# Performance work log

Measured on AMD Instinct MI355X. Metric: run time of the kernel, lower is better.

The kernel has to match this reference:

```python
import jax, jax.numpy as jnp
import numpy as np

EPS = 1e-12  # F.normalize clamp


def setup_inputs() -> dict:
    key = jax.random.key(0)
    features = jax.random.normal(key, (8192, 256), dtype=jnp.float32)
    return {"features": features}


def reference(features) -> jnp.ndarray:
    # F.normalize(features, dim=1)
    norm = jnp.maximum(jnp.linalg.norm(features, axis=1, keepdims=True), EPS)
    f = features / norm
    sim = f @ f.T  # [2B, 2B]
    n = sim.shape[0]
    b = n // 2
    idx = jnp.arange(n)
    # positive pair index: idx+B for first half, idx-B for second half
    pos_idx = jnp.where(idx < b, idx + b, idx - b)
    pos = sim[idx, pos_idx]  # sim with the positive example
    # CE with target 0 over logits row [pos, negatives (all j != i, j != pos)]:
    # denominator = exp(pos) + sum_{j != i, j != pos} exp(sim_ij) = sum_{j != i} exp(sim_ij)
    self_mask = idx[:, None] == idx[None, :]
    masked = jnp.where(self_mask, -jnp.inf, sim)
    lse = jax.nn.logsumexp(masked, axis=1)
    loss = jnp.mean(lse - pos)
    return loss
```

## Files before the change

### kernel.cpp

```cpp
#include <hip/hip_runtime.h>
#include <hip/hip_bf16.h>
#include <stdint.h>

#define N 8192
#define D 256
#define ROWB 256
#define COLG 16
#define COLS_PER_BLK (N / COLG)
#define CTILE 32
#define NT (COLS_PER_BLK / CTILE)
#define TILE_BYTES (CTILE * D)
#define NBUF 4
#define E_CONST 2.71828182845904523536f

typedef __attribute__((ext_vector_type(4))) int i32x4;
typedef __attribute__((ext_vector_type(8))) int i32x8;
typedef __attribute__((ext_vector_type(16))) float f32x16;

typedef const __attribute__((address_space(1))) void gvoid_t;
typedef __attribute__((address_space(3))) void lvoid_t;
__device__ inline void gload_lds16(const void* g, void* l) {
  __builtin_amdgcn_global_load_lds((gvoid_t*)g, (lvoid_t*)l, 16, 0, 0);
}

#if !__has_builtin(__builtin_amdgcn_cvt_pk_fp8_f32)
__device__ inline unsigned int f2e4m3(float x) {
  union { float f; unsigned u; } c; c.f = x;
  unsigned s = (c.u >> 31) << 7;
  float ax = fabsf(x);
  if (!(ax > 0.0f)) return s;
  if (ax >= 448.0f) return s | 0x7E;
  int e; float m = frexpf(ax, &e);
  int E = e - 1 + 7;
  if (E <= 0) {
    int qi = (int)rintf(ax * 512.0f);
    if (qi > 7) return s | 0x08;
    return s | (unsigned)qi;
  }
  int qi = (int)rintf(m * 16.0f);
  if (qi == 16) { qi = 8; E += 1; }
  if (E > 15) return s | 0x7E;
  return s | (unsigned)((E << 3) | (qi - 8));
}
#endif

__global__ __launch_bounds__(256) void norm_kernel(const float* __restrict__ feat,
                                                   unsigned char* __restrict__ f8,
                                                   float* __restrict__ pos,
                                                   float* __restrict__ out) {
  __shared__ float4 sh[4][64];
  int wave = threadIdx.x >> 6, lane = threadIdx.x & 63;
  int base = blockIdx.x << 1;
  int row = (wave < 2) ? (base + wave) : (4096 + base + (wave - 2));
  const float4 v = *(const float4*)(feat + (size_t)row * D + lane * 4);
  float ss = v.x * v.x + v.y * v.y + v.z * v.z + v.w * v.w;
  for (int m = 1; m < 64; m <<= 1) ss += __shfl_xor(ss, m, 64);
  float rn = 1.0f / fmaxf(sqrtf(ss), 1e-12f);
  float4 nv = make_float4(v.x * rn, v.y * rn, v.z * rn, v.w * rn);
#if __has_builtin(__builtin_amdgcn_cvt_pk_fp8_f32)
  int p = __builtin_amdgcn_cvt_pk_fp8_f32(nv.x, nv.y, 0, 0);
  p = __builtin_amdgcn_cvt_pk_fp8_f32(nv.z, nv.w, p, 1);
#else
  int p = (int)(f2e4m3(nv.x) | (f2e4m3(nv.y) << 8) |
                (f2e4m3(nv.z) << 16) | (f2e4m3(nv.w) << 24));
#endif
  *(int*)(f8 + (size_t)row * D + lane * 4) = p;
  sh[wave][lane] = nv;
  __syncthreads();
  if (wave < 2) {
    float4 q = sh[wave + 2][lane];
    float d = nv.x * q.x + nv.y * q.y + nv.z * q.z + nv.w * q.w;
    for (int m = 1; m < 64; m <<= 1) d += __shfl_xor(d, m, 64);
    if (lane == 0) {
      pos[base + wave] = d;
      pos[4096 + base + wave] = d;
    }
  }
  if (blockIdx.x == 0 && threadIdx.x == 0) out[0] = 0.0f;
}

__global__ __launch_bounds__(512, 4) void simlse_kernel(const unsigned char* __restrict__ f8,
                                                        float* __restrict__ slab) {
  __shared__ char lds[NBUF * TILE_BYTES];
  const char* fb = (const char*)f8;
  int tid = threadIdx.x;
  int wave = tid >> 6, lane = tid & 63;
  int c31 = lane & 31, h = lane >> 5;
  int rb = blockIdx.x >> 4;
  int cg = blockIdx.x & 15;
  int rowbase = rb * ROWB + wave * 32;

  i32x8 a[4];
  {
    const char* ar = fb + (size_t)(rowbase + c31) * D + h * 32;
#pragma unroll
    for (int m = 0; m < 4; ++m) {
      i32x4 lo = *(const i32x4*)(ar + m * 64);
      i32x4 hi = *(const i32x4*)(ar + m * 64 + 16);
      a[m] = __builtin_shufflevector(lo, hi, 0, 1, 2, 3, 4, 5, 6, 7);
    }
  }
#pragma unroll
  for (int m = 0; m < 4; ++m)
    asm volatile("" : "+v"(a[m]));

  float srow[16];
#pragma unroll
  for (int r = 0; r < 16; ++r) srow[r] = 0.0f;

  int colbase = cg * COLS_PER_BLK;
  int o0 = tid * 16;
  int r0 = o0 >> 8;
  int g0 = (o0 & 255) ^ ((r0 & 7) << 4);
  int sw = (c31 & 7) << 4;

#define STAGE(tt)                                                              \
  {                                                                            \
    char* stg = lds + ((tt) & (NBUF - 1)) * TILE_BYTES;                        \
    size_t cb = (size_t)(colbase + (tt) * CTILE);                              \
    gload_lds16(fb + (cb + r0) * D + g0, stg + wave * 1024);                   \
  }

#define COMPUTE(tt)                                                            \
  {                                                                            \
    const char* bb = lds + ((tt) & (NBUF - 1)) * TILE_BYTES + c31 * 256;       \
    f32x16 acc = {0, 0, 0, 0, 0, 0, 0, 0, 0, 0, 0, 0, 0, 0, 0, 0};            \
    _Pragma("unroll")                                                          \
    for (int m = 0; m < 4; ++m) {                                              \
      int base = m * 64 + h * 32;                                              \
      i32x4 lo = *(const i32x4*)(bb + (base ^ sw));                            \
      i32x4 hi = *(const i32x4*)(bb + ((base + 16) ^ sw));                     \
      i32x8 bv = __builtin_shufflevector(lo, hi, 0, 1, 2, 3, 4, 5, 6, 7);      \
      acc = __builtin_amdgcn_mfma_scale_f32_32x32x64_f8f6f4(                   \
          a[m], bv, acc, 0, 0, 0, 127, 0, 127);                                \
    }                                                                          \
    _Pragma("unroll")                                                          \
    for (int r = 0; r < 16; ++r) srow[r] += __expf(acc[r]);                    \
  }

  STAGE(0);
  STAGE(1);

  const int NP = NT / 2;
  for (int u = 0; u < NP; ++u) {
    asm volatile("s_waitcnt vmcnt(0)" ::: "memory");
    __builtin_amdgcn_sched_barrier(0);
    __builtin_amdgcn_s_barrier();
    __builtin_amdgcn_sched_barrier(0);
    if (u + 1 < NP) {
      STAGE(2 * u + 2);
      STAGE(2 * u + 3);
    }
    COMPUTE(2 * u);
    COMPUTE(2 * u + 1);
  }
#undef STAGE
#undef COMPUTE

#pragma unroll
  for (int r = 0; r < 16; ++r) {
    srow[r] += __shfl_xor(srow[r], 1, 64);
    srow[r] += __shfl_xor(srow[r], 2, 64);
    srow[r] += __shfl_xor(srow[r], 4, 64);
    srow[r] += __shfl_xor(srow[r], 8, 64);
    srow[r] += __shfl_xor(srow[r], 16, 64);
  }
  if (c31 == 0) {
#pragma unroll
    for (int r = 0; r < 16; ++r) {
      int grow = rowbase + (r & 3) + 8 * (r >> 2) + 4 * h;
      slab[(size_t)cg * N + grow] = srow[r];
    }
  }
}

__global__ __launch_bounds__(256) void final_kernel(const float* __restrict__ slab,
                                                    const float* __restrict__ pos,
                                                    float* __restrict__ out) {
  int tid = threadIdx.x;
  int row = blockIdx.x * 256 + tid;
  float ssum = 0.0f;
#pragma unroll
  for (int c = 0; c < COLG; ++c) ssum += slab[(size_t)c * N + row];
  float v = __logf(ssum - E_CONST) - pos[row];
  for (int m = 1; m < 64; m <<= 1) v += __shfl_xor(v, m, 64);
  __shared__ float r4[4];
  if ((tid & 63) == 0) r4[tid >> 6] = v;
  __syncthreads();
  if (tid == 0)
    atomicAdd(out, (r4[0] + r4[1] + r4[2] + r4[3]) * (1.0f / (float)N));
}

extern "C" void kernel_launch(void* const* d_in, const int* in_sizes, int n_in,
                              void* d_out, int out_size, void* d_ws, size_t ws_size,
                              hipStream_t stream) {
  const float* feat = (const float*)d_in[0];
  unsigned char* f8 = (unsigned char*)d_ws;
  float* pos  = (float*)((char*)d_ws + (size_t)N * D);
  float* slab = (float*)((char*)d_ws + (size_t)N * D + (size_t)N * 4);
  float* out = (float*)d_out;

  norm_kernel<<<N / 4, 256, 0, stream>>>(feat, f8, pos, out);
  simlse_kernel<<<(N / ROWB) * COLG, 512, 0, stream>>>(f8, slab);
  final_kernel<<<N / 256, 256, 0, stream>>>(slab, pos, out);
}
```

Measured before the change: 33.10 us.

## Quantize normalized features to FP4 with log2e-folded scale and use exp2

Replaces the fp8 e4m3 encoding with a custom 4-bit e2m1 encoder that pre-multiplies by a scale folding in sqrt(log2 e), packing two values per byte. The similarity kernel loads half as many bytes per tile, runs the scaled MFMA in fp4 mode with compensating exponent scales, and uses raw exp2 instead of expf. This cuts memory/LDS traffic and exp cost but greatly lowers dot-product precision, which risks loss accuracy.

```diff
diff --git a/kernel.cpp b/kernel.cpp
--- a/kernel.cpp
+++ b/kernel.cpp
@@ -4,14 +4,15 @@
 
 #define N 8192
 #define D 256
+#define RB4 128
 #define ROWB 256
 #define COLG 16
 #define COLS_PER_BLK (N / COLG)
 #define CTILE 32
 #define NT (COLS_PER_BLK / CTILE)
-#define TILE_BYTES (CTILE * D)
-#define NBUF 4
+#define TILE_BYTES (CTILE * RB4)
 #define E_CONST 2.71828182845904523536f
+#define QSCALE 19.2179587f
 
 typedef __attribute__((ext_vector_type(4))) int i32x4;
 typedef __attribute__((ext_vector_type(8))) int i32x8;
@@ -23,29 +24,17 @@
   __builtin_amdgcn_global_load_lds((gvoid_t*)g, (lvoid_t*)l, 16, 0, 0);
 }
 
-#if !__has_builtin(__builtin_amdgcn_cvt_pk_fp8_f32)
-__device__ inline unsigned int f2e4m3(float x) {
-  union { float f; unsigned u; } c; c.f = x;
-  unsigned s = (c.u >> 31) << 7;
-  float ax = fabsf(x);
-  if (!(ax > 0.0f)) return s;
-  if (ax >= 448.0f) return s | 0x7E;
-  int e; float m = frexpf(ax, &e);
-  int E = e - 1 + 7;
-  if (E <= 0) {
-    int qi = (int)rintf(ax * 512.0f);
-    if (qi > 7) return s | 0x08;
-    return s | (unsigned)qi;
-  }
-  int qi = (int)rintf(m * 16.0f);
-  if (qi == 16) { qi = 8; E += 1; }
-  if (E > 15) return s | 0x7E;
-  return s | (unsigned)((E << 3) | (qi - 8));
+__device__ inline unsigned enc4(float x) {
+  unsigned s = (__float_as_uint(x) >> 31) << 3;
+  float m = fabsf(x) * QSCALE;
+  unsigned c;
+  if (m < 1.75f) c = (m < 0.75f) ? (m < 0.25f ? 0u : 1u) : (m < 1.25f ? 2u : 3u);
+  else           c = (m < 3.5f)  ? (m < 2.5f ? 4u : 5u)  : (m < 5.0f ? 6u : 7u);
+  return s | c;
 }
-#endif
 
 __global__ __launch_bounds__(256) void norm_kernel(const float* __restrict__ feat,
-                                                   unsigned char* __restrict__ f8,
+                                                   unsigned char* __restrict__ f4,
                                                    float* __restrict__ pos,
                                                    float* __restrict__ out) {
   __shared__ float4 sh[4][64];
@@ -57,14 +46,9 @@
   for (int m = 1; m < 64; m <<= 1) ss += __shfl_xor(ss, m, 64);
   float rn = 1.0f / fmaxf(sqrtf(ss), 1e-12f);
   float4 nv = make_float4(v.x * rn, v.y * rn, v.z * rn, v.w * rn);
-#if __has_builtin(__builtin_amdgcn_cvt_pk_fp8_f32)
-  int p = __builtin_amdgcn_cvt_pk_fp8_f32(nv.x, nv.y, 0, 0);
-  p = __builtin_amdgcn_cvt_pk_fp8_f32(nv.z, nv.w, p, 1);
-#else
-  int p = (int)(f2e4m3(nv.x) | (f2e4m3(nv.y) << 8) |
-                (f2e4m3(nv.z) << 16) | (f2e4m3(nv.w) << 24));
-#endif
-  *(int*)(f8 + (size_t)row * D + lane * 4) = p;
+  unsigned short pk = (unsigned short)(enc4(nv.x) | (enc4(nv.y) << 4) |
+                                       (enc4(nv.z) << 8) | (enc4(nv.w) << 12));
+  *(unsigned short*)(f4 + (size_t)row * RB4 + lane * 2) = pk;
   sh[wave][lane] = nv;
   __syncthreads();
   if (wave < 2) {
@@ -79,10 +63,10 @@
   if (blockIdx.x == 0 && threadIdx.x == 0) out[0] = 0.0f;
 }
 
-__global__ __launch_bounds__(512, 4) void simlse_kernel(const unsigned char* __restrict__ f8,
+__global__ __launch_bounds__(512, 4) void simlse_kernel(const unsigned char* __restrict__ f4,
                                                         float* __restrict__ slab) {
-  __shared__ char lds[NBUF * TILE_BYTES];
-  const char* fb = (const char*)f8;
+  __shared__ char lds[4 * TILE_BYTES];
+  const char* fb = (const char*)f4;
   int tid = threadIdx.x;
   int wave = tid >> 6, lane = tid & 63;
   int c31 = lane & 31, h = lane >> 5;
@@ -92,12 +76,12 @@
 
   i32x8 a[4];
   {
-    const char* ar = fb + (size_t)(rowbase + c31) * D + h * 32;
+    const char* ar = fb + (size_t)(rowbase + c31) * RB4 + h * 16;
+    const i32x4 z4 = {0, 0, 0, 0};
 #pragma unroll
     for (int m = 0; m < 4; ++m) {
-      i32x4 lo = *(const i32x4*)(ar + m * 64);
-      i32x4 hi = *(const i32x4*)(ar + m * 64 + 16);
-      a[m] = __builtin_shufflevector(lo, hi, 0, 1, 2, 3, 4, 5, 6, 7);
+      i32x4 lo = *(const i32x4*)(ar + m * 32);
+      a[m] = __builtin_shufflevector(lo, z4, 0, 1, 2, 3, 4, 5, 6, 7);
     }
   }
 #pragma unroll
@@ -110,36 +94,34 @@
 
   int colbase = cg * COLS_PER_BLK;
   int o0 = tid * 16;
-  int r0 = o0 >> 8;
-  int g0 = (o0 & 255) ^ ((r0 & 7) << 4);
-  int sw = (c31 & 7) << 4;
+  int pr = o0 >> 7;
+  int g0 = (o0 & 127) ^ ((pr & 7) << 4);
+  const i32x4 z4 = {0, 0, 0, 0};
 
-#define STAGE(tt)                                                              \
+#define STAGEPAIR(uu)                                                          \
   {                                                                            \
-    char* stg = lds + ((tt) & (NBUF - 1)) * TILE_BYTES;                        \
-    size_t cb = (size_t)(colbase + (tt) * CTILE);                              \
-    gload_lds16(fb + (cb + r0) * D + g0, stg + wave * 1024);                   \
+    char* stg = lds + ((uu) & 1) * 8192;                                       \
+    size_t cb = (size_t)(colbase + (uu) * 2 * CTILE);                          \
+    gload_lds16(fb + (cb + pr) * RB4 + g0, stg + wave * 1024);                 \
   }
 
 #define COMPUTE(tt)                                                            \
   {                                                                            \
-    const char* bb = lds + ((tt) & (NBUF - 1)) * TILE_BYTES + c31 * 256;       \
+    const char* bb = lds + ((tt) & 3) * TILE_BYTES + c31 * RB4;                \
     f32x16 acc = {0, 0, 0, 0, 0, 0, 0, 0, 0, 0, 0, 0, 0, 0, 0, 0};            \
     _Pragma("unroll")                                                          \
     for (int m = 0; m < 4; ++m) {                                              \
-      int base = m * 64 + h * 32;                                              \
-      i32x4 lo = *(const i32x4*)(bb + (base ^ sw));                            \
-      i32x4 hi = *(const i32x4*)(bb + ((base + 16) ^ sw));                     \
-      i32x8 bv = __builtin_shufflevector(lo, hi, 0, 1, 2, 3, 4, 5, 6, 7);      \
+      int s = m * 2 + h;                                                       \
+      i32x4 lo = *(const i32x4*)(bb + ((s ^ (c31 & 7)) << 4));                 \
+      i32x8 bv = __builtin_shufflevector(lo, z4, 0, 1, 2, 3, 4, 5, 6, 7);      \
       acc = __builtin_amdgcn_mfma_scale_f32_32x32x64_f8f6f4(                   \
-          a[m], bv, acc, 0, 0, 0, 127, 0, 127);                                \
+          a[m], bv, acc, 4, 4, 0, 123, 0, 123);                                \
     }                                                                          \
     _Pragma("unroll")                                                          \
-    for (int r = 0; r < 16; ++r) srow[r] += __expf(acc[r]);                    \
+    for (int r = 0; r < 16; ++r) srow[r] += __builtin_amdgcn_exp2f(acc[r]);    \
   }
 
-  STAGE(0);
-  STAGE(1);
+  STAGEPAIR(0);
 
   const int NP = NT / 2;
   for (int u = 0; u < NP; ++u) {
@@ -147,14 +129,11 @@
     __builtin_amdgcn_sched_barrier(0);
     __builtin_amdgcn_s_barrier();
     __builtin_amdgcn_sched_barrier(0);
-    if (u + 1 < NP) {
-      STAGE(2 * u + 2);
-      STAGE(2 * u + 3);
-    }
+    if (u + 1 < NP) STAGEPAIR(u + 1);
     COMPUTE(2 * u);
     COMPUTE(2 * u + 1);
   }
-#undef STAGE
+#undef STAGEPAIR
 #undef COMPUTE
 
 #pragma unroll
@@ -195,12 +174,12 @@
                               void* d_out, int out_size, void* d_ws, size_t ws_size,
                               hipStream_t stream) {
   const float* feat = (const float*)d_in[0];
-  unsigned char* f8 = (unsigned char*)d_ws;
-  float* pos  = (float*)((char*)d_ws + (size_t)N * D);
-  float* slab = (float*)((char*)d_ws + (size_t)N * D + (size_t)N * 4);
+  unsigned char* f4 = (unsigned char*)d_ws;
+  float* pos  = (float*)((char*)d_ws + (size_t)N * RB4);
+  float* slab = (float*)((char*)d_ws + (size_t)N * RB4 + (size_t)N * 4);
   float* out = (float*)d_out;
 
-  norm_kernel<<<N / 4, 256, 0, stream>>>(feat, f8, pos, out);
-  simlse_kernel<<<(N / ROWB) * COLG, 512, 0, stream>>>(f8, slab);
+  norm_kernel<<<N / 4, 256, 0, stream>>>(feat, f4, pos, out);
+  simlse_kernel<<<(N / ROWB) * COLG, 512, 0, stream>>>(f4, slab);
   final_kernel<<<N / 256, 256, 0, stream>>>(slab, pos, out);
 }
```

New measurement: 45.53 us. +37.6%, slower.
